# Performance work log

Measured on AMD Instinct MI355X. Metric: run time of the kernel, lower is better.

## Reference

```python
import jax, jax.numpy as jnp
import numpy as np

ARRAY_SIZE = 128   # crossbar rows
CBITS = 4          # psum ADC bits
LEV = 2 ** (CBITS - 1)
ALPHA = ARRAY_SIZE / LEV   # psum quant step
EPS = 1e-5

# ---- binary activation / weight quant with STE (hardtanh grad) ----
@jax.custom_vjp
def ste_sign(x):
    return jnp.where(x >= 0, 1.0, -1.0).astype(x.dtype)

def _sign_fwd(x):
    return ste_sign(x), x

def _sign_bwd(x, g):
    return (g * (jnp.abs(x) <= 1.0).astype(g.dtype),)

ste_sign.defvjp(_sign_fwd, _sign_bwd)

# ---- psum (partial-sum) quantization: cbits-level ADC over each crossbar array ----
@jax.custom_vjp
def psum_quant(p):
    return jnp.clip(jnp.round(p / ALPHA), -LEV, LEV - 1) * ALPHA

def _pq_fwd(p):
    return psum_quant(p), p

def _pq_bwd(p, g):
    return (g * (jnp.abs(p) <= ARRAY_SIZE).astype(g.dtype),)

psum_quant.defvjp(_pq_fwd, _pq_bwd)

# ---- layers ----
def bn(x, p):
    g, b, m, v = p  # each [C]
    sh = (1, -1) + (1,) * (x.ndim - 2)
    return (x - m.reshape(sh)) * (g.reshape(sh) / jnp.sqrt(v.reshape(sh) + EPS)) + b.reshape(sh)

def maxpool2(x):
    return jax.lax.reduce_window(x, -jnp.inf, jax.lax.max, (1, 1, 2, 2), (1, 1, 2, 2), 'VALID')

def conv_same(x, w):
    return jax.lax.conv_general_dilated(x, w, (1, 1), 'SAME')

def psum_conv(x, w):
    # crossbar-mapped conv: input channels split into groups of arraySize//(kh*kw),
    # each group conv'd separately, psum-quantized (ADC), then accumulated.
    O, Cin, kh, kw = w.shape
    chunk = max(1, ARRAY_SIZE // (kh * kw))
    G = -(-Cin // chunk)
    pad = G * chunk - Cin
    xp = jnp.pad(x, ((0, 0), (0, pad), (0, 0), (0, 0)))
    wp = jnp.pad(w, ((0, 0), (0, pad), (0, 0), (0, 0)))
    B, _, H, W = x.shape
    xg = xp.reshape(B, G, chunk, H, W).transpose(1, 0, 2, 3, 4)   # [G,B,c,H,W]
    wg = wp.reshape(O, G, chunk, kh, kw).transpose(1, 0, 2, 3, 4)  # [G,O,c,kh,kw]
    ps = jax.vmap(conv_same)(xg, wg)                               # [G,B,O,H,W]
    return psum_quant(ps).sum(0)

def psum_linear(x, w):
    # x [B,D], w [O,D]; D divisible by ARRAY_SIZE
    B, D = x.shape
    O = w.shape[0]
    G = D // ARRAY_SIZE
    ps = jnp.einsum('bgc,ogc->gbo', x.reshape(B, G, ARRAY_SIZE), w.reshape(O, G, ARRAY_SIZE))
    return psum_quant(ps).sum(0)


def setup_inputs() -> dict:
    key = jax.random.key(0)
    ks = iter(jax.random.split(key, 64))
    def nrm(shape, s=0.05):
        return jax.random.normal(next(ks), shape, jnp.float32) * s
    def bnp(C):
        return jnp.stack([jax.random.uniform(next(ks), (C,), jnp.float32) + 0.5,
                          nrm((C,), 0.1), nrm((C,), 0.1),
                          jax.random.uniform(next(ks), (C,), jnp.float32) + 0.5])
    return dict(
        x=jax.random.normal(next(ks), (64, 3, 32, 32), jnp.float32),
        conv0_w=nrm((128, 3, 3, 3)), bn0=bnp(128),
        w1=nrm((128, 128, 3, 3)), bn1=bnp(128),
        w2=nrm((256, 128, 3, 3)), bn2=bnp(256),
        w3=nrm((256, 256, 3, 3)), bn3=bnp(256),
        w4=nrm((512, 256, 3, 3)), bn4=bnp(512),
        w5=nrm((512, 512, 3, 3)), bn5=bnp(512),
        fc1_w=nrm((1024, 8192)), bnf1=bnp(1024),
        fc2_w=nrm((1024, 1024)), bnf2=bnp(1024),
        out_w=nrm((10, 1024)), out_b=nrm((10,)), bnout=bnp(10),
    )


def reference(x, conv0_w, bn0, w1, bn1, w2, bn2, w3, bn3, w4, bn4, w5, bn5,
              fc1_w, bnf1, fc2_w, bnf2, out_w, out_b, bnout):
    h = conv_same(x, conv0_w)                       # full-precision first conv
    h = ste_sign(bn(h, bn0))
    h = psum_conv(h, ste_sign(w1)); h = maxpool2(h); h = ste_sign(bn(h, bn1))
    h = psum_conv(h, ste_sign(w2)); h = ste_sign(bn(h, bn2))
    h = psum_conv(h, ste_sign(w3)); h = maxpool2(h); h = ste_sign(bn(h, bn3))
    h = psum_conv(h, ste_sign(w4)); h = ste_sign(bn(h, bn4))
    h = psum_conv(h, ste_sign(w5)); h = maxpool2(h); h = ste_sign(bn(h, bn5))
    h = h.reshape(h.shape[0], -1)                   # [B, 8192]
    h = ste_sign(bn(psum_linear(h, ste_sign(fc1_w)), bnf1))
    h = bn(psum_linear(h, ste_sign(fc2_w)), bnf2)   # abits=32 -> identity nonlinear
    h = h @ out_w.T + out_b
    return bn(h, bnout)
```

## Files before the change

kernel.cpp:

```cpp
#include <hip/hip_runtime.h>
#include <cstdint>
#include <cstddef>

using bf16x8 = __attribute__((ext_vector_type(8))) short;
using f32x4  = __attribute__((ext_vector_type(4))) float;
using u32x4  = __attribute__((ext_vector_type(4))) unsigned int;

#define DI __device__ __forceinline__

DI float pq16(float ps) {
    float q = rintf(ps * 0.0625f);
    q = fminf(7.f, fmaxf(-8.f, q));
    return q * 16.f;
}

DI float bnv(float x, float g, float b, float m, float v) {
    return (x - m) * (g / sqrtf(v + 1e-5f)) + b;
}

DI unsigned short sgn_bf16(float v) {
    return (v >= 0.f) ? (unsigned short)0x3F80 : (unsigned short)0xBF80;
}

__global__ __launch_bounds__(256)
void k_conv0(const float* __restrict__ x, const float* __restrict__ w,
             const float* __restrict__ bnp, unsigned short* __restrict__ out) {
    __shared__ float sX[3][3][36];
    const int b = blockIdx.x >> 5, y = blockIdx.x & 31;
    const int tid = threadIdx.x;
    const int o = tid & 127, xc = tid >> 7;

    for (int i = tid; i < 3 * 3 * 36; i += 256) {
        int col = i % 36, rr = (i / 36) % 3, c = i / 108;
        int gy = y + rr - 1, gx = col - 1;
        float v = 0.f;
        if ((unsigned)gy < 32u && (unsigned)gx < 32u)
            v = x[((b * 3 + c) * 32 + gy) * 32 + gx];
        sX[c][rr][col] = v;
    }
    float wr[27];
    const float* wp = w + o * 27;
    #pragma unroll
    for (int t = 0; t < 27; ++t) wr[t] = wp[t];
    __syncthreads();

    const float bg = bnp[o], bb = bnp[128 + o], bm = bnp[256 + o], bv = bnp[384 + o];
    unsigned short* op = out + ((size_t)(b * 32 + y) * 32) * 128 + o;

    #pragma unroll
    for (int q = 0; q < 4; ++q) {
        float acc0 = 0.f, acc1 = 0.f, acc2 = 0.f, acc3 = 0.f;
        const int X0 = xc * 16 + q * 4;
        #pragma unroll
        for (int c = 0; c < 3; ++c)
            #pragma unroll
            for (int ky = 0; ky < 3; ++ky) {
                float xv0 = sX[c][ky][X0 + 0], xv1 = sX[c][ky][X0 + 1];
                float xv2 = sX[c][ky][X0 + 2], xv3 = sX[c][ky][X0 + 3];
                float xv4 = sX[c][ky][X0 + 4], xv5 = sX[c][ky][X0 + 5];
                float w0 = wr[c * 9 + ky * 3 + 0];
                float w1 = wr[c * 9 + ky * 3 + 1];
                float w2 = wr[c * 9 + ky * 3 + 2];
                acc0 += xv0 * w0 + xv1 * w1 + xv2 * w2;
                acc1 += xv1 * w0 + xv2 * w1 + xv3 * w2;
                acc2 += xv2 * w0 + xv3 * w1 + xv4 * w2;
                acc3 += xv3 * w0 + xv4 * w1 + xv5 * w2;
            }
        op[(size_t)(X0 + 0) * 128] = sgn_bf16(bnv(acc0, bg, bb, bm, bv));
        op[(size_t)(X0 + 1) * 128] = sgn_bf16(bnv(acc1, bg, bb, bm, bv));
        op[(size_t)(X0 + 2) * 128] = sgn_bf16(bnv(acc2, bg, bb, bm, bv));
        op[(size_t)(X0 + 3) * 128] = sgn_bf16(bnv(acc3, bg, bb, bm, bv));
    }
}

__global__ __launch_bounds__(256)
void k_pack_w(const float* __restrict__ w, unsigned short* __restrict__ wpk,
              int Cin, int O, int G) {
    int idx = blockIdx.x * 256 + threadIdx.x;
    int total = G * O * 160;
    if (idx >= total) return;
    int c = idx & 15;
    int tap = (idx >> 4) % 10;
    int rest = idx / 160;
    int o = rest % O, g = rest / O;
    unsigned short v = 0;
    int cg = g * 14 + c;
    if (tap < 9 && c < 14 && cg < Cin)
        v = sgn_bf16(w[((size_t)o * Cin + cg) * 9 + tap]);
    wpk[idx] = v;
}

template <int H, int W, int Cin, int O, int G, int RH, int RW, int POOLMODE>
__global__ __launch_bounds__(256)
void k_conv_mfma(const unsigned int* __restrict__ act,
                 const unsigned short* __restrict__ wpk,
                 const float* __restrict__ bnp,
                 unsigned short* __restrict__ outa,
                 unsigned short* __restrict__ a5p) {
    constexpr int SH = RH + 2, SW = RW + 2;
    constexpr int MS = RH * RW / 16;
    constexpr int NREGX = W / RW;
    static_assert(POOLMODE != 1 || RW == 16, "pool mode 1 needs RW=16");
    static_assert(POOLMODE != 2 || (RW == 8 && MS == 4), "pool mode 2 needs 8x8");

    __shared__ __align__(16) unsigned int sA[SH * SW * 12];

    const int tid  = threadIdx.x;
    const int regY = (int)blockIdx.x / NREGX, regX = (int)blockIdx.x % NREGX;
    const int o0   = blockIdx.y * 64;
    const int b    = blockIdx.z;

    const int lane = tid & 63, wv = tid >> 6;
    const int n  = lane & 15;
    const int kb = lane >> 4;
    const int hb = kb >> 1, ch = kb & 1;

    int baseA[MS];
    #pragma unroll
    for (int ms = 0; ms < MS; ++ms) {
        int p = ms * 16 + n;
        int y = p / RW, x = p % RW;
        baseA[ms] = (y * SW + x) * 48 + ch * 16;
    }

    float tot[MS][4];
    #pragma unroll
    for (int ms = 0; ms < MS; ++ms) {
        tot[ms][0] = 0.f; tot[ms][1] = 0.f; tot[ms][2] = 0.f; tot[ms][3] = 0.f;
    }

    const unsigned short* wrow = wpk + ((size_t)o0 + wv * 16 + n) * 160 + ch * 8;

    #pragma unroll 1
    for (int g = 0; g < G; ++g) {
        const int rem_dw = (Cin - g * 14) >> 1;
        for (int i = tid; i < SH * SW * 8; i += 256) {
            int cp = i & 7, slot = i >> 3;
            int yy = slot / SW, xx = slot - yy * SW;
            int gy = regY * RH + yy - 1, gx = regX * RW + xx - 1;
            unsigned int v = 0;
            if (cp < 7 && cp < rem_dw &&
                (unsigned)gy < (unsigned)H && (unsigned)gx < (unsigned)W)
                v = act[(((size_t)b * H + gy) * W + gx) * (Cin / 2) + g * 7 + cp];
            sA[slot * 12 + cp] = v;
        }
        const unsigned short* wg = wrow + (size_t)g * O * 160;
        bf16x8 bq[5];
        #pragma unroll
        for (int s = 0; s < 5; ++s) {
            int tap = 2 * s + hb;
            bq[s] = *(const bf16x8*)(wg + tap * 16);
        }
        __syncthreads();

        const char* sAc = (const char*)sA;
        #pragma unroll
        for (int ms = 0; ms < MS; ++ms) {
            f32x4 acc = {0.f, 0.f, 0.f, 0.f};
            #pragma unroll
            for (int s = 0; s < 5; ++s) {
                const int t0 = 2 * s, t1 = 2 * s + 1;
                const int off0 = ((t0 / 3) * SW + (t0 % 3)) * 48;
                const int off1 = (t1 >= 9) ? 0 : ((t1 / 3) * SW + (t1 % 3)) * 48;
                int off = hb ? off1 : off0;
                bf16x8 af = *(const bf16x8*)(sAc + baseA[ms] + off);
                acc = __builtin_amdgcn_mfma_f32_16x16x32_bf16(af, bq[s], acc, 0, 0, 0);
            }
            tot[ms][0] += pq16(acc[0]);
            tot[ms][1] += pq16(acc[1]);
            tot[ms][2] += pq16(acc[2]);
            tot[ms][3] += pq16(acc[3]);
        }
        __syncthreads();
    }

    const int oc = o0 + wv * 16 + n;
    const float bg = bnp[oc], bb = bnp[O + oc], bm = bnp[2 * O + oc], bvr = bnp[3 * O + oc];

    if constexpr (POOLMODE == 0) {
        #pragma unroll
        for (int ms = 0; ms < MS; ++ms)
            #pragma unroll
            for (int r = 0; r < 4; ++r) {
                int p = ms * 16 + 4 * kb + r;
                int y = regY * RH + p / RW, x = regX * RW + p % RW;
                float val = bnv(tot[ms][r], bg, bb, bm, bvr);
                outa[(((size_t)b * H + y) * W + x) * O + oc] = sgn_bf16(val);
            }
    } else if constexpr (POOLMODE == 1) {
        #pragma unroll
        for (int j = 0; j < MS / 2; ++j)
            #pragma unroll
            for (int q = 0; q < 2; ++q) {
                float v = fmaxf(fmaxf(tot[2 * j][2 * q], tot[2 * j][2 * q + 1]),
                                fmaxf(tot[2 * j + 1][2 * q], tot[2 * j + 1][2 * q + 1]));
                float val = bnv(v, bg, bb, bm, bvr);
                int py = regY * (RH / 2) + j, px = regX * (RW / 2) + 2 * kb + q;
                outa[(((size_t)b * (H / 2) + py) * (W / 2) + px) * O + oc] = sgn_bf16(val);
            }
    } else {
        #pragma unroll
        for (int ms = 0; ms < MS; ++ms)
            #pragma unroll
            for (int q = 0; q < 2; ++q) {
                float h = fmaxf(tot[ms][2 * q], tot[ms][2 * q + 1]);
                float o2 = __shfl_xor(h, 32);
                float v = fmaxf(h, o2);
                if (hb == 0) {
                    float val = bnv(v, bg, bb, bm, bvr);
                    int d = oc * 16 + ms * 4 + 2 * ch + q;
                    a5p[((size_t)(d >> 3) * 64 + b) * 8 + (d & 7)] = sgn_bf16(val);
                }
            }
    }
}

template <int D, int GPB>
__global__ __launch_bounds__(256)
void k_fc_mfma(const unsigned short* __restrict__ bpk, const float* __restrict__ w,
               float* __restrict__ accg) {
    const int lane = threadIdx.x & 63, wv = threadIdx.x >> 6;
    const int n = lane & 15, kb = lane >> 4;
    const int orow = blockIdx.x * 64 + wv * 16 + n;
    const int g0 = blockIdx.y * GPB;

    float tot[4][4];
    #pragma unroll
    for (int s = 0; s < 4; ++s)
        #pragma unroll
        for (int r = 0; r < 4; ++r) tot[s][r] = 0.f;

    #pragma unroll 1
    for (int g = 0; g < GPB; ++g) {
        const int kbase = (g0 + g) * 128;
        f32x4 a0 = {0,0,0,0}, a1 = {0,0,0,0}, a2 = {0,0,0,0}, a3 = {0,0,0,0};
        #pragma unroll
        for (int s = 0; s < 4; ++s) {
            const int k0 = kbase + s * 32 + kb * 8;
            const float* wp = w + (size_t)orow * D + k0;
            float4 wlo = *(const float4*)wp;
            float4 whi = *(const float4*)(wp + 4);
            bf16x8 af;
            af[0] = (short)sgn_bf16(wlo.x); af[1] = (short)sgn_bf16(wlo.y);
            af[2] = (short)sgn_bf16(wlo.z); af[3] = (short)sgn_bf16(wlo.w);
            af[4] = (short)sgn_bf16(whi.x); af[5] = (short)sgn_bf16(whi.y);
            af[6] = (short)sgn_bf16(whi.z); af[7] = (short)sgn_bf16(whi.w);
            const unsigned short* bp = bpk + (size_t)(k0 >> 3) * 512;
            bf16x8 b0 = *(const bf16x8*)(bp + (n +  0) * 8);
            bf16x8 b1 = *(const bf16x8*)(bp + (n + 16) * 8);
            bf16x8 b2 = *(const bf16x8*)(bp + (n + 32) * 8);
            bf16x8 b3 = *(const bf16x8*)(bp + (n + 48) * 8);
            a0 = __builtin_amdgcn_mfma_f32_16x16x32_bf16(af, b0, a0, 0, 0, 0);
            a1 = __builtin_amdgcn_mfma_f32_16x16x32_bf16(af, b1, a1, 0, 0, 0);
            a2 = __builtin_amdgcn_mfma_f32_16x16x32_bf16(af, b2, a2, 0, 0, 0);
            a3 = __builtin_amdgcn_mfma_f32_16x16x32_bf16(af, b3, a3, 0, 0, 0);
        }
        #pragma unroll
        for (int r = 0; r < 4; ++r) {
            tot[0][r] += pq16(a0[r]); tot[1][r] += pq16(a1[r]);
            tot[2][r] += pq16(a2[r]); tot[3][r] += pq16(a3[r]);
        }
    }
    const int od = blockIdx.x * 64 + wv * 16 + kb * 4;
    #pragma unroll
    for (int s = 0; s < 4; ++s)
        #pragma unroll
        for (int r = 0; r < 4; ++r)
            atomicAdd(&accg[(size_t)(od + r) * 64 + s * 16 + n], tot[s][r]);
}

template <bool SIGN>
__global__ __launch_bounds__(256)
void k_fc_ep(const float* __restrict__ accg, const float* __restrict__ bnp,
             unsigned short* __restrict__ packed, float* __restrict__ h2, int O) {
    int idx = blockIdx.x * 256 + threadIdx.x;
    int b = idx & 63, o = idx >> 6;
    float val = bnv(accg[idx], bnp[o], bnp[O + o], bnp[2 * O + o], bnp[3 * O + o]);
    if (SIGN) packed[((size_t)(o >> 3) * 64 + b) * 8 + (o & 7)] = sgn_bf16(val);
    else      h2[(size_t)b * 1024 + o] = val;
}

__global__ __launch_bounds__(64)
void k_out(const float* __restrict__ h2, const float* __restrict__ ow,
           const float* __restrict__ ob, const float* __restrict__ bnp,
           float* __restrict__ out) {
    int b = blockIdx.x / 10, o = blockIdx.x % 10;
    int lane = threadIdx.x;
    float acc = 0.f;
    #pragma unroll
    for (int i = 0; i < 16; ++i) {
        int k = i * 64 + lane;
        acc += h2[b * 1024 + k] * ow[o * 1024 + k];
    }
    #pragma unroll
    for (int off = 32; off; off >>= 1) acc += __shfl_xor(acc, off);
    if (lane == 0)
        out[b * 10 + o] = bnv(acc + ob[o], bnp[o], bnp[10 + o], bnp[20 + o], bnp[30 + o]);
}

extern "C" void kernel_launch(void* const* d_in, const int* in_sizes, int n_in,
                              void* d_out, int out_size, void* d_ws, size_t ws_size,
                              hipStream_t stream) {
    const float* x     = (const float*)d_in[0];
    const float* w0    = (const float*)d_in[1];
    const float* bn0   = (const float*)d_in[2];
    const float* w1    = (const float*)d_in[3];
    const float* bn1   = (const float*)d_in[4];
    const float* w2    = (const float*)d_in[5];
    const float* bn2   = (const float*)d_in[6];
    const float* w3    = (const float*)d_in[7];
    const float* bn3   = (const float*)d_in[8];
    const float* w4    = (const float*)d_in[9];
    const float* bn4   = (const float*)d_in[10];
    const float* w5    = (const float*)d_in[11];
    const float* bn5   = (const float*)d_in[12];
    const float* fc1w  = (const float*)d_in[13];
    const float* bnf1  = (const float*)d_in[14];
    const float* fc2w  = (const float*)d_in[15];
    const float* bnf2  = (const float*)d_in[16];
    const float* outw  = (const float*)d_in[17];
    const float* outb  = (const float*)d_in[18];
    const float* bnout = (const float*)d_in[19];

    char* ws = (char*)d_ws;
    unsigned short* actA  = (unsigned short*)(ws);
    unsigned short* actB  = (unsigned short*)(ws + 16777216);
    unsigned short* wpk   = (unsigned short*)(ws + 20971520);
    unsigned short* a5p   = (unsigned short*)(ws + 27262976);
    unsigned short* a6p   = (unsigned short*)(ws + 28311552);
    float*          h1acc = (float*)(ws + 28442624);
    float*          h2acc = (float*)(ws + 28704768);
    float*          h2    = (float*)(ws + 28966912);

    const unsigned int* actA32 = (const unsigned int*)actA;
    const unsigned int* actB32 = (const unsigned int*)actB;

    hipMemsetAsync(h1acc, 0, 262144, stream);
    hipMemsetAsync(h2acc, 0, 262144, stream);

    k_conv0<<<dim3(2048), dim3(256), 0, stream>>>(x, w0, bn0, actA);

    k_pack_w<<<dim3(800), dim3(256), 0, stream>>>(w1, wpk, 128, 128, 10);
    k_conv_mfma<32, 32, 128, 128, 10, 8, 16, 1>
        <<<dim3(8, 2, 64), dim3(256), 0, stream>>>(actA32, wpk, bn1, actB, nullptr);

    k_pack_w<<<dim3(1600), dim3(256), 0, stream>>>(w2, wpk, 128, 256, 10);
    k_conv_mfma<16, 16, 128, 256, 10, 8, 16, 0>
        <<<dim3(2, 4, 64), dim3(256), 0, stream>>>(actB32, wpk, bn2, actA, nullptr);

    k_pack_w<<<dim3(3040), dim3(256), 0, stream>>>(w3, wpk, 256, 256, 19);
    k_conv_mfma<16, 16, 256, 256, 19, 8, 16, 1>
        <<<dim3(2, 4, 64), dim3(256), 0, stream>>>(actA32, wpk, bn3, actB, nullptr);

    k_pack_w<<<dim3(6080), dim3(256), 0, stream>>>(w4, wpk, 256, 512, 19);
    k_conv_mfma<8, 8, 256, 512, 19, 8, 8, 0>
        <<<dim3(1, 8, 64), dim3(256), 0, stream>>>(actB32, wpk, bn4, actA, nullptr);

    k_pack_w<<<dim3(11840), dim3(256), 0, stream>>>(w5, wpk, 512, 512, 37);
    k_conv_mfma<8, 8, 512, 512, 37, 8, 8, 2>
        <<<dim3(1, 8, 64), dim3(256), 0, stream>>>(actA32, wpk, bn5, nullptr, a5p);

    k_fc_mfma<8192, 4><<<dim3(16, 16), dim3(256), 0, stream>>>(a5p, fc1w, h1acc);
    k_fc_ep<true><<<dim3(256), dim3(256), 0, stream>>>(h1acc, bnf1, a6p, nullptr, 1024);

    k_fc_mfma<1024, 1><<<dim3(16, 8), dim3(256), 0, stream>>>(a6p, fc2w, h2acc);
    k_fc_ep<false><<<dim3(256), dim3(256), 0, stream>>>(h2acc, bnf2, nullptr, h2, 1024);

    k_out<<<dim3(640), dim3(64), 0, stream>>>(h2, outw, outb, bnout, (float*)d_out);
}
```

Before: 298.2 us.

## Split-K conv4/conv5 over crossbar groups with atomics, smaller tiles for conv2/conv3

Conv4 and conv5 now split their crossbar-group loop into chunks across extra blocks. Each chunk accumulates psum-quantized partials into a float buffer with atomicAdd, and separate epilogue kernels apply BN and sign, plus maxpool and packing for conv5. Conv2 and conv3 switch to 8x8 tiles, with conv3 gaining a new in-kernel 8x8 pooling mode, and FC1 uses finer group splitting. This raises block counts on the small-spatial layers to fill more compute units, at the cost of atomics, memsets of the partial buffer and extra epilogue launches.

```diff
diff --git a/kernel.cpp b/kernel.cpp
--- a/kernel.cpp
+++ b/kernel.cpp
@@ -90,25 +90,32 @@
     wpk[idx] = v;
 }
 
-template <int H, int W, int Cin, int O, int G, int RH, int RW, int POOLMODE>
+template <int H, int W, int Cin, int O, int RH, int RW, int POOLMODE>
 __global__ __launch_bounds__(256)
 void k_conv_mfma(const unsigned int* __restrict__ act,
                  const unsigned short* __restrict__ wpk,
                  const float* __restrict__ bnp,
                  unsigned short* __restrict__ outa,
-                 unsigned short* __restrict__ a5p) {
+                 unsigned short* __restrict__ a5p,
+                 float* __restrict__ Pacc,
+                 int gsz, int Gtot) {
     constexpr int SH = RH + 2, SW = RW + 2;
     constexpr int MS = RH * RW / 16;
     constexpr int NREGX = W / RW;
+    constexpr int NTILES = (H / RH) * (W / RW);
     static_assert(POOLMODE != 1 || RW == 16, "pool mode 1 needs RW=16");
-    static_assert(POOLMODE != 2 || (RW == 8 && MS == 4), "pool mode 2 needs 8x8");
+    static_assert((POOLMODE != 2 && POOLMODE != 4) || (RW == 8 && MS == 4), "modes 2/4 need 8x8");
 
     __shared__ __align__(16) unsigned int sA[SH * SW * 12];
 
     const int tid  = threadIdx.x;
-    const int regY = (int)blockIdx.x / NREGX, regX = (int)blockIdx.x % NREGX;
+    const int bx   = (int)blockIdx.x;
+    const int tile = bx % NTILES, chunk = bx / NTILES;
+    const int regY = tile / NREGX, regX = tile % NREGX;
     const int o0   = blockIdx.y * 64;
     const int b    = blockIdx.z;
+    const int g0   = chunk * gsz;
+    const int gend = min(g0 + gsz, Gtot);
 
     const int lane = tid & 63, wv = tid >> 6;
     const int n  = lane & 15;
@@ -132,7 +139,7 @@
     const unsigned short* wrow = wpk + ((size_t)o0 + wv * 16 + n) * 160 + ch * 8;
 
     #pragma unroll 1
-    for (int g = 0; g < G; ++g) {
+    for (int g = g0; g < gend; ++g) {
         const int rem_dw = (Cin - g * 14) >> 1;
         for (int i = tid; i < SH * SW * 8; i += 256) {
             int cp = i & 7, slot = i >> 3;
@@ -175,6 +182,19 @@
     }
 
     const int oc = o0 + wv * 16 + n;
+
+    if constexpr (POOLMODE == 3) {
+        #pragma unroll
+        for (int ms = 0; ms < MS; ++ms)
+            #pragma unroll
+            for (int r = 0; r < 4; ++r) {
+                int p = ms * 16 + 4 * kb + r;
+                int y = regY * RH + p / RW, x = regX * RW + p % RW;
+                atomicAdd(&Pacc[(((size_t)b * H + y) * W + x) * O + oc], tot[ms][r]);
+            }
+        return;
+    }
+
     const float bg = bnp[oc], bb = bnp[O + oc], bm = bnp[2 * O + oc], bvr = bnp[3 * O + oc];
 
     if constexpr (POOLMODE == 0) {
@@ -208,11 +228,40 @@
                 float v = fmaxf(h, o2);
                 if (hb == 0) {
                     float val = bnv(v, bg, bb, bm, bvr);
-                    int d = oc * 16 + ms * 4 + 2 * ch + q;
-                    a5p[((size_t)(d >> 3) * 64 + b) * 8 + (d & 7)] = sgn_bf16(val);
+                    int py = ms, px = 2 * ch + q;
+                    if constexpr (POOLMODE == 2) {
+                        int d = oc * 16 + py * 4 + px;
+                        a5p[((size_t)(d >> 3) * 64 + b) * 8 + (d & 7)] = sgn_bf16(val);
+                    } else {
+                        int gpy = regY * (RH / 2) + py, gpx = regX * (RW / 2) + px;
+                        outa[(((size_t)b * (H / 2) + gpy) * (W / 2) + gpx) * O + oc] = sgn_bf16(val);
+                    }
                 }
             }
     }
+}
+
+template <int O>
+__global__ __launch_bounds__(256)
+void k_ep_bnsign(const float* __restrict__ P, const float* __restrict__ bnp,
+                 unsigned short* __restrict__ outa) {
+    int idx = blockIdx.x * 256 + threadIdx.x;
+    int o = idx & (O - 1);
+    float val = bnv(P[idx], bnp[o], bnp[O + o], bnp[2 * O + o], bnp[3 * O + o]);
+    outa[idx] = sgn_bf16(val);
+}
+
+__global__ __launch_bounds__(256)
+void k_ep_pool_pack(const float* __restrict__ P, const float* __restrict__ bnp,
+                    unsigned short* __restrict__ a5p) {
+    int idx = blockIdx.x * 256 + threadIdx.x;
+    int o = idx & 511;
+    int px = (idx >> 9) & 3, py = (idx >> 11) & 3, b = idx >> 13;
+    const float* base = P + (((size_t)b * 8 + 2 * py) * 8 + 2 * px) * 512 + o;
+    float v = fmaxf(fmaxf(base[0], base[512]), fmaxf(base[8 * 512], base[8 * 512 + 512]));
+    float val = bnv(v, bnp[o], bnp[512 + o], bnp[1024 + o], bnp[1536 + o]);
+    int d = o * 16 + py * 4 + px;
+    a5p[((size_t)(d >> 3) * 64 + b) * 8 + (d & 7)] = sgn_bf16(val);
 }
 
 template <int D, int GPB>
@@ -326,11 +375,12 @@
     unsigned short* actA  = (unsigned short*)(ws);
     unsigned short* actB  = (unsigned short*)(ws + 16777216);
     unsigned short* wpk   = (unsigned short*)(ws + 20971520);
-    unsigned short* a5p   = (unsigned short*)(ws + 27262976);
-    unsigned short* a6p   = (unsigned short*)(ws + 28311552);
-    float*          h1acc = (float*)(ws + 28442624);
-    float*          h2acc = (float*)(ws + 28704768);
-    float*          h2    = (float*)(ws + 28966912);
+    float*          P     = (float*)(ws + 27262976);
+    unsigned short* a5p   = (unsigned short*)(ws + 35651584);
+    unsigned short* a6p   = (unsigned short*)(ws + 36700160);
+    float*          h1acc = (float*)(ws + 36831232);
+    float*          h2acc = (float*)(ws + 37093376);
+    float*          h2    = (float*)(ws + 37355520);
 
     const unsigned int* actA32 = (const unsigned int*)actA;
     const unsigned int* actB32 = (const unsigned int*)actB;
@@ -341,26 +391,30 @@
     k_conv0<<<dim3(2048), dim3(256), 0, stream>>>(x, w0, bn0, actA);
 
     k_pack_w<<<dim3(800), dim3(256), 0, stream>>>(w1, wpk, 128, 128, 10);
-    k_conv_mfma<32, 32, 128, 128, 10, 8, 16, 1>
-        <<<dim3(8, 2, 64), dim3(256), 0, stream>>>(actA32, wpk, bn1, actB, nullptr);
+    k_conv_mfma<32, 32, 128, 128, 8, 16, 1>
+        <<<dim3(8, 2, 64), dim3(256), 0, stream>>>(actA32, wpk, bn1, actB, nullptr, nullptr, 10, 10);
 
     k_pack_w<<<dim3(1600), dim3(256), 0, stream>>>(w2, wpk, 128, 256, 10);
-    k_conv_mfma<16, 16, 128, 256, 10, 8, 16, 0>
-        <<<dim3(2, 4, 64), dim3(256), 0, stream>>>(actB32, wpk, bn2, actA, nullptr);
+    k_conv_mfma<16, 16, 128, 256, 8, 8, 0>
+        <<<dim3(4, 4, 64), dim3(256), 0, stream>>>(actB32, wpk, bn2, actA, nullptr, nullptr, 10, 10);
 
     k_pack_w<<<dim3(3040), dim3(256), 0, stream>>>(w3, wpk, 256, 256, 19);
-    k_conv_mfma<16, 16, 256, 256, 19, 8, 16, 1>
-        <<<dim3(2, 4, 64), dim3(256), 0, stream>>>(actA32, wpk, bn3, actB, nullptr);
+    k_conv_mfma<16, 16, 256, 256, 8, 8, 4>
+        <<<dim3(4, 4, 64), dim3(256), 0, stream>>>(actA32, wpk, bn3, actB, nullptr, nullptr, 19, 19);
 
     k_pack_w<<<dim3(6080), dim3(256), 0, stream>>>(w4, wpk, 256, 512, 19);
-    k_conv_mfma<8, 8, 256, 512, 19, 8, 8, 0>
-        <<<dim3(1, 8, 64), dim3(256), 0, stream>>>(actB32, wpk, bn4, actA, nullptr);
+    hipMemsetAsync(P, 0, 8388608, stream);
+    k_conv_mfma<8, 8, 256, 512, 8, 8, 3>
+        <<<dim3(4, 8, 64), dim3(256), 0, stream>>>(actB32, wpk, nullptr, nullptr, nullptr, P, 5, 19);
+    k_ep_bnsign<512><<<dim3(8192), dim3(256), 0, stream>>>(P, bn4, actA);
 
     k_pack_w<<<dim3(11840), dim3(256), 0, stream>>>(w5, wpk, 512, 512, 37);
-    k_conv_mfma<8, 8, 512, 512, 37, 8, 8, 2>
-        <<<dim3(1, 8, 64), dim3(256), 0, stream>>>(actA32, wpk, bn5, nullptr, a5p);
-
-    k_fc_mfma<8192, 4><<<dim3(16, 16), dim3(256), 0, stream>>>(a5p, fc1w, h1acc);
+    hipMemsetAsync(P, 0, 8388608, stream);
+    k_conv_mfma<8, 8, 512, 512, 8, 8, 3>
+        <<<dim3(4, 8, 64), dim3(256), 0, stream>>>(actA32, wpk, nullptr, nullptr, nullptr, P, 10, 37);
+    k_ep_pool_pack<<<dim3(2048), dim3(256), 0, stream>>>(P, bn5, a5p);
+
+    k_fc_mfma<8192, 1><<<dim3(16, 64), dim3(256), 0, stream>>>(a5p, fc1w, h1acc);
     k_fc_ep<true><<<dim3(256), dim3(256), 0, stream>>>(h1acc, bnf1, a6p, nullptr, 1024);
 
     k_fc_mfma<1024, 1><<<dim3(16, 8), dim3(256), 0, stream>>>(a6p, fc2w, h2acc);
```

Result: slower. 321.1 us (+7.7%).

## Restructure binary convs to batch-as-M MFMA with blocked channel layout

Applied to the files above, without the earlier changes.

Replaces the spatial-tile conv kernel with one that maps batch into the MFMA M dimension and uses a channel-block-major activation layout, so each block loads fragments straight from global memory with no shared-memory staging or barriers. Each wave computes four 16-output tiles, which raises reuse of weight fragments. Weights are pre-scaled by 1/16 so the psum quant becomes a rint plus clamp, with the 16x folded into the epilogue. The last conv writes raw floats and a separate pool/BN kernel packs them for fc1, and fc1 is split into more groups. In exchange it uses more registers, adds an extra kernel and buffer, and reads activations directly from global memory where the shared-memory tiling used to provide reuse.

```diff
diff --git a/kernel.cpp b/kernel.cpp
--- a/kernel.cpp
+++ b/kernel.cpp
@@ -4,22 +4,18 @@
 
 using bf16x8 = __attribute__((ext_vector_type(8))) short;
 using f32x4  = __attribute__((ext_vector_type(4))) float;
-using u32x4  = __attribute__((ext_vector_type(4))) unsigned int;
 
 #define DI __device__ __forceinline__
-
-DI float pq16(float ps) {
-    float q = rintf(ps * 0.0625f);
-    q = fminf(7.f, fmaxf(-8.f, q));
-    return q * 16.f;
-}
 
 DI float bnv(float x, float g, float b, float m, float v) {
     return (x - m) * (g / sqrtf(v + 1e-5f)) + b;
 }
-
 DI unsigned short sgn_bf16(float v) {
     return (v >= 0.f) ? (unsigned short)0x3F80 : (unsigned short)0xBF80;
+}
+DI float pq_scaled(float a) {
+    float q = rintf(a);
+    return fminf(7.f, fmaxf(-8.f, q));
 }
 
 __global__ __launch_bounds__(256)
@@ -45,7 +41,10 @@
     __syncthreads();
 
     const float bg = bnp[o], bb = bnp[128 + o], bm = bnp[256 + o], bv = bnp[384 + o];
-    unsigned short* op = out + ((size_t)(b * 32 + y) * 32) * 128 + o;
+    const int cb0 = (o / 14) * 2 + ((o % 14) >> 3);
+    const int sl0 = (o % 14) & 7;
+    unsigned short* op = out + (size_t)(y * 32) * 10240 + (size_t)cb0 * 512
+                             + (size_t)b * 8 + sl0;
 
     #pragma unroll
     for (int q = 0; q < 4; ++q) {
@@ -66,10 +65,10 @@
                 acc2 += xv2 * w0 + xv3 * w1 + xv4 * w2;
                 acc3 += xv3 * w0 + xv4 * w1 + xv5 * w2;
             }
-        op[(size_t)(X0 + 0) * 128] = sgn_bf16(bnv(acc0, bg, bb, bm, bv));
-        op[(size_t)(X0 + 1) * 128] = sgn_bf16(bnv(acc1, bg, bb, bm, bv));
-        op[(size_t)(X0 + 2) * 128] = sgn_bf16(bnv(acc2, bg, bb, bm, bv));
-        op[(size_t)(X0 + 3) * 128] = sgn_bf16(bnv(acc3, bg, bb, bm, bv));
+        op[(size_t)(X0 + 0) * 10240] = sgn_bf16(bnv(acc0, bg, bb, bm, bv));
+        op[(size_t)(X0 + 1) * 10240] = sgn_bf16(bnv(acc1, bg, bb, bm, bv));
+        op[(size_t)(X0 + 2) * 10240] = sgn_bf16(bnv(acc2, bg, bb, bm, bv));
+        op[(size_t)(X0 + 3) * 10240] = sgn_bf16(bnv(acc3, bg, bb, bm, bv));
     }
 }
 
@@ -77,142 +76,156 @@
 void k_pack_w(const float* __restrict__ w, unsigned short* __restrict__ wpk,
               int Cin, int O, int G) {
     int idx = blockIdx.x * 256 + threadIdx.x;
-    int total = G * O * 160;
-    if (idx >= total) return;
-    int c = idx & 15;
-    int tap = (idx >> 4) % 10;
-    int rest = idx / 160;
-    int o = rest % O, g = rest / O;
+    if (idx >= G * O * 160) return;
+    int c8 = idx & 7;
+    int o  = (idx >> 3) % O;
+    int r2 = (idx >> 3) / O;
+    int chdw = r2 & 1, tap = (r2 >> 1) % 10, g = r2 / 20;
+    int c = chdw * 8 + c8, cg = g * 14 + c;
     unsigned short v = 0;
-    int cg = g * 14 + c;
     if (tap < 9 && c < 14 && cg < Cin)
-        v = sgn_bf16(w[((size_t)o * Cin + cg) * 9 + tap]);
+        v = (w[((size_t)o * Cin + cg) * 9 + tap] >= 0.f) ? (unsigned short)0x3D80
+                                                         : (unsigned short)0xBD80;
     wpk[idx] = v;
 }
 
-template <int H, int W, int Cin, int O, int G, int RH, int RW, int POOLMODE>
-__global__ __launch_bounds__(256)
-void k_conv_mfma(const unsigned int* __restrict__ act,
-                 const unsigned short* __restrict__ wpk,
-                 const float* __restrict__ bnp,
-                 unsigned short* __restrict__ outa,
-                 unsigned short* __restrict__ a5p) {
-    constexpr int SH = RH + 2, SW = RW + 2;
-    constexpr int MS = RH * RW / 16;
-    constexpr int NREGX = W / RW;
-    static_assert(POOLMODE != 1 || RW == 16, "pool mode 1 needs RW=16");
-    static_assert(POOLMODE != 2 || (RW == 8 && MS == 4), "pool mode 2 needs 8x8");
-
-    __shared__ __align__(16) unsigned int sA[SH * SW * 12];
-
-    const int tid  = threadIdx.x;
-    const int regY = (int)blockIdx.x / NREGX, regX = (int)blockIdx.x % NREGX;
-    const int o0   = blockIdx.y * 64;
-    const int b    = blockIdx.z;
-
-    const int lane = tid & 63, wv = tid >> 6;
-    const int n  = lane & 15;
-    const int kb = lane >> 4;
-    const int hb = kb >> 1, ch = kb & 1;
-
-    int baseA[MS];
+template <int H, int W, int CB, int O, int G, int MS, int OUTMODE, int OUTCB, int MINW>
+__global__ __launch_bounds__(256, MINW)
+void k_conv_bm(const char* __restrict__ act, const char* __restrict__ wpk,
+               const float* __restrict__ bnp, unsigned short* __restrict__ outa,
+               float* __restrict__ P) {
+    static_assert(OUTMODE != 1 || MS == 4, "pool mode needs quad");
+    const int tid = threadIdx.x;
+    const int lane = tid & 63, bg = tid >> 6;
+    const int n = lane & 15, kb = lane >> 4, hb = kb >> 1, chdw = kb & 1;
+    const int sp = blockIdx.x;
+    const int o0 = blockIdx.y * 64;
+
+    int pix[MS];
+    int qY = 0, qX = 0;
+    if constexpr (MS == 4) {
+        qY = sp / (W / 2); qX = sp % (W / 2);
+        #pragma unroll
+        for (int ms = 0; ms < 4; ++ms)
+            pix[ms] = (2 * qY + (ms >> 1)) * W + 2 * qX + (ms & 1);
+    } else {
+        pix[0] = sp;
+    }
+
+    const int bl = (bg * 16 + n) * 16 + chdw * 1024;
+    int off[MS][5];
     #pragma unroll
     for (int ms = 0; ms < MS; ++ms) {
-        int p = ms * 16 + n;
-        int y = p / RW, x = p % RW;
-        baseA[ms] = (y * SW + x) * 48 + ch * 16;
-    }
-
-    float tot[MS][4];
-    #pragma unroll
-    for (int ms = 0; ms < MS; ++ms) {
-        tot[ms][0] = 0.f; tot[ms][1] = 0.f; tot[ms][2] = 0.f; tot[ms][3] = 0.f;
-    }
-
-    const unsigned short* wrow = wpk + ((size_t)o0 + wv * 16 + n) * 160 + ch * 8;
+        int py = pix[ms] / W, px = pix[ms] % W;
+        #pragma unroll
+        for (int s = 0; s < 5; ++s) {
+            int t = 2 * s + hb;
+            int ty = t / 3, tx = t - 3 * ty;
+            int gy = py + ty - 1, gx = px + tx - 1;
+            bool valid = (t <= 8) && ((unsigned)gy < (unsigned)H) && ((unsigned)gx < (unsigned)W);
+            off[ms][s] = valid ? ((gy * W + gx) * CB) * 1024 + bl : (int)0xC0000000;
+        }
+    }
+
+    const char* wl = wpk + (size_t)(((hb * 2 + chdw) * O) + o0 + n) * 16;
+
+    float tot[MS][4][4];
+    #pragma unroll
+    for (int ms = 0; ms < MS; ++ms)
+        #pragma unroll
+        for (int nt = 0; nt < 4; ++nt)
+            #pragma unroll
+            for (int r = 0; r < 4; ++r) tot[ms][nt][r] = 0.f;
+
+    const bf16x8 az = {0, 0, 0, 0, 0, 0, 0, 0};
 
     #pragma unroll 1
     for (int g = 0; g < G; ++g) {
-        const int rem_dw = (Cin - g * 14) >> 1;
-        for (int i = tid; i < SH * SW * 8; i += 256) {
-            int cp = i & 7, slot = i >> 3;
-            int yy = slot / SW, xx = slot - yy * SW;
-            int gy = regY * RH + yy - 1, gx = regX * RW + xx - 1;
-            unsigned int v = 0;
-            if (cp < 7 && cp < rem_dw &&
-                (unsigned)gy < (unsigned)H && (unsigned)gx < (unsigned)W)
-                v = act[(((size_t)b * H + gy) * W + gx) * (Cin / 2) + g * 7 + cp];
-            sA[slot * 12 + cp] = v;
-        }
-        const unsigned short* wg = wrow + (size_t)g * O * 160;
-        bf16x8 bq[5];
+        f32x4 acc[MS][4];
+        #pragma unroll
+        for (int ms = 0; ms < MS; ++ms)
+            #pragma unroll
+            for (int nt = 0; nt < 4; ++nt) acc[ms][nt] = (f32x4){0.f, 0.f, 0.f, 0.f};
+
+        const char* wg = wl + (size_t)g * (20 * O * 16);
+        const char* ag = act + (size_t)g * 2048;
         #pragma unroll
         for (int s = 0; s < 5; ++s) {
-            int tap = 2 * s + hb;
-            bq[s] = *(const bf16x8*)(wg + tap * 16);
-        }
-        __syncthreads();
-
-        const char* sAc = (const char*)sA;
-        #pragma unroll
-        for (int ms = 0; ms < MS; ++ms) {
-            f32x4 acc = {0.f, 0.f, 0.f, 0.f};
-            #pragma unroll
-            for (int s = 0; s < 5; ++s) {
-                const int t0 = 2 * s, t1 = 2 * s + 1;
-                const int off0 = ((t0 / 3) * SW + (t0 % 3)) * 48;
-                const int off1 = (t1 >= 9) ? 0 : ((t1 / 3) * SW + (t1 % 3)) * 48;
-                int off = hb ? off1 : off0;
-                bf16x8 af = *(const bf16x8*)(sAc + baseA[ms] + off);
-                acc = __builtin_amdgcn_mfma_f32_16x16x32_bf16(af, bq[s], acc, 0, 0, 0);
+            bf16x8 bq[4];
+            #pragma unroll
+            for (int nt = 0; nt < 4; ++nt)
+                bq[nt] = *(const bf16x8*)(wg + s * (4 * O * 16) + nt * 256);
+            #pragma unroll
+            for (int ms = 0; ms < MS; ++ms) {
+                bf16x8 af = az;
+                int ofs = off[ms][s];
+                if (ofs >= 0) af = *(const bf16x8*)(ag + ofs);
+                #pragma unroll
+                for (int nt = 0; nt < 4; ++nt)
+                    acc[ms][nt] = __builtin_amdgcn_mfma_f32_16x16x32_bf16(af, bq[nt], acc[ms][nt], 0, 0, 0);
             }
-            tot[ms][0] += pq16(acc[0]);
-            tot[ms][1] += pq16(acc[1]);
-            tot[ms][2] += pq16(acc[2]);
-            tot[ms][3] += pq16(acc[3]);
-        }
-        __syncthreads();
-    }
-
-    const int oc = o0 + wv * 16 + n;
-    const float bg = bnp[oc], bb = bnp[O + oc], bm = bnp[2 * O + oc], bvr = bnp[3 * O + oc];
-
-    if constexpr (POOLMODE == 0) {
+        }
         #pragma unroll
         for (int ms = 0; ms < MS; ++ms)
             #pragma unroll
+            for (int nt = 0; nt < 4; ++nt)
+                #pragma unroll
+                for (int r = 0; r < 4; ++r)
+                    tot[ms][nt][r] += pq_scaled(acc[ms][nt][r]);
+    }
+
+    const int bb = bg * 16 + kb * 4;
+    if constexpr (OUTMODE == 2) {
+        #pragma unroll
+        for (int nt = 0; nt < 4; ++nt) {
+            int oc = o0 + nt * 16 + n;
+            #pragma unroll
+            for (int r = 0; r < 4; ++r)
+                P[((size_t)pix[0] * 512 + oc) * 64 + bb + r] = tot[0][nt][r];
+        }
+    } else {
+        #pragma unroll
+        for (int nt = 0; nt < 4; ++nt) {
+            int oc = o0 + nt * 16 + n;
+            float g_ = bnp[oc], b_ = bnp[O + oc], m_ = bnp[2 * O + oc], v_ = bnp[3 * O + oc];
+            int q14 = oc / 14, r14 = oc - 14 * q14;
+            int cb = 2 * q14 + (r14 >> 3), sl = r14 & 7;
+            int ppos = (OUTMODE == 1) ? (qY * (W / 2) + qX) : pix[0];
+            #pragma unroll
             for (int r = 0; r < 4; ++r) {
-                int p = ms * 16 + 4 * kb + r;
-                int y = regY * RH + p / RW, x = regX * RW + p % RW;
-                float val = bnv(tot[ms][r], bg, bb, bm, bvr);
-                outa[(((size_t)b * H + y) * W + x) * O + oc] = sgn_bf16(val);
+                float v;
+                if constexpr (OUTMODE == 1)
+                    v = fmaxf(fmaxf(tot[0][nt][r], tot[1][nt][r]),
+                              fmaxf(tot[2][nt][r], tot[3][nt][r]));
+                else
+                    v = tot[0][nt][r];
+                float val = bnv(16.f * v, g_, b_, m_, v_);
+                outa[((size_t)ppos * OUTCB + cb) * 512 + (size_t)(bb + r) * 8 + sl] = sgn_bf16(val);
             }
-    } else if constexpr (POOLMODE == 1) {
-        #pragma unroll
-        for (int j = 0; j < MS / 2; ++j)
-            #pragma unroll
-            for (int q = 0; q < 2; ++q) {
-                float v = fmaxf(fmaxf(tot[2 * j][2 * q], tot[2 * j][2 * q + 1]),
-                                fmaxf(tot[2 * j + 1][2 * q], tot[2 * j + 1][2 * q + 1]));
-                float val = bnv(v, bg, bb, bm, bvr);
-                int py = regY * (RH / 2) + j, px = regX * (RW / 2) + 2 * kb + q;
-                outa[(((size_t)b * (H / 2) + py) * (W / 2) + px) * O + oc] = sgn_bf16(val);
-            }
-    } else {
-        #pragma unroll
-        for (int ms = 0; ms < MS; ++ms)
-            #pragma unroll
-            for (int q = 0; q < 2; ++q) {
-                float h = fmaxf(tot[ms][2 * q], tot[ms][2 * q + 1]);
-                float o2 = __shfl_xor(h, 32);
-                float v = fmaxf(h, o2);
-                if (hb == 0) {
-                    float val = bnv(v, bg, bb, bm, bvr);
-                    int d = oc * 16 + ms * 4 + 2 * ch + q;
-                    a5p[((size_t)(d >> 3) * 64 + b) * 8 + (d & 7)] = sgn_bf16(val);
-                }
-            }
-    }
+        }
+    }
+}
+
+__global__ __launch_bounds__(256)
+void k_ep_pool5(const float* __restrict__ P, const float* __restrict__ bnp,
+                unsigned short* __restrict__ a5p) {
+    int idx = blockIdx.x * 256 + threadIdx.x;
+    int b = idx & 63;
+    int o = (idx >> 6) & 511;
+    int pq = idx >> 15;
+    int py = pq >> 2, px = pq & 3;
+    const float* p0 = P + ((size_t)(2 * py * 8 + 2 * px) * 512 + o) * 64 + b;
+    const int dx = 512 * 64, dy = 8 * 512 * 64;
+    float v = fmaxf(fmaxf(p0[0], p0[dx]), fmaxf(p0[dy], p0[dy + dx]));
+    float val = bnv(16.f * v, bnp[o], bnp[512 + o], bnp[1024 + o], bnp[1536 + o]);
+    int d = o * 16 + py * 4 + px;
+    a5p[((size_t)(d >> 3) * 64 + b) * 8 + (d & 7)] = sgn_bf16(val);
+}
+
+DI float pq16(float ps) {
+    float q = rintf(ps * 0.0625f);
+    q = fminf(7.f, fmaxf(-8.f, q));
+    return q * 16.f;
 }
 
 template <int D, int GPB>
@@ -323,48 +336,46 @@
     const float* bnout = (const float*)d_in[19];
 
     char* ws = (char*)d_ws;
-    unsigned short* actA  = (unsigned short*)(ws);
-    unsigned short* actB  = (unsigned short*)(ws + 16777216);
-    unsigned short* wpk   = (unsigned short*)(ws + 20971520);
-    unsigned short* a5p   = (unsigned short*)(ws + 27262976);
-    unsigned short* a6p   = (unsigned short*)(ws + 28311552);
-    float*          h1acc = (float*)(ws + 28442624);
-    float*          h2acc = (float*)(ws + 28704768);
-    float*          h2    = (float*)(ws + 28966912);
-
-    const unsigned int* actA32 = (const unsigned int*)actA;
-    const unsigned int* actB32 = (const unsigned int*)actB;
+    char*           ping  = ws;
+    char*           pong  = ws + 20971520;
+    unsigned short* wpk   = (unsigned short*)(ws + 26214400);
+    float*          P     = (float*)(ws + 32505856);
+    unsigned short* a5p   = (unsigned short*)(ws + 40894464);
+    unsigned short* a6p   = (unsigned short*)(ws + 41943040);
+    float*          h1acc = (float*)(ws + 42074112);
+    float*          h2acc = (float*)(ws + 42336256);
+    float*          h2    = (float*)(ws + 42598400);
+    const char*     wpkc  = (const char*)wpk;
 
     hipMemsetAsync(h1acc, 0, 262144, stream);
     hipMemsetAsync(h2acc, 0, 262144, stream);
 
-    k_conv0<<<dim3(2048), dim3(256), 0, stream>>>(x, w0, bn0, actA);
+    k_conv0<<<dim3(2048), dim3(256), 0, stream>>>(x, w0, bn0, (unsigned short*)ping);
 
     k_pack_w<<<dim3(800), dim3(256), 0, stream>>>(w1, wpk, 128, 128, 10);
-    k_conv_mfma<32, 32, 128, 128, 10, 8, 16, 1>
-        <<<dim3(8, 2, 64), dim3(256), 0, stream>>>(actA32, wpk, bn1, actB, nullptr);
+    k_conv_bm<32, 32, 20, 128, 10, 4, 1, 20, 2>
+        <<<dim3(256, 2), dim3(256), 0, stream>>>(ping, wpkc, bn1, (unsigned short*)pong, nullptr);
 
     k_pack_w<<<dim3(1600), dim3(256), 0, stream>>>(w2, wpk, 128, 256, 10);
-    k_conv_mfma<16, 16, 128, 256, 10, 8, 16, 0>
-        <<<dim3(2, 4, 64), dim3(256), 0, stream>>>(actB32, wpk, bn2, actA, nullptr);
+    k_conv_bm<16, 16, 20, 256, 10, 1, 0, 38, 4>
+        <<<dim3(256, 4), dim3(256), 0, stream>>>(pong, wpkc, bn2, (unsigned short*)ping, nullptr);
 
     k_pack_w<<<dim3(3040), dim3(256), 0, stream>>>(w3, wpk, 256, 256, 19);
-    k_conv_mfma<16, 16, 256, 256, 19, 8, 16, 1>
-        <<<dim3(2, 4, 64), dim3(256), 0, stream>>>(actA32, wpk, bn3, actB, nullptr);
+    k_conv_bm<16, 16, 38, 256, 19, 4, 1, 38, 2>
+        <<<dim3(64, 4), dim3(256), 0, stream>>>(ping, wpkc, bn3, (unsigned short*)pong, nullptr);
 
     k_pack_w<<<dim3(6080), dim3(256), 0, stream>>>(w4, wpk, 256, 512, 19);
-    k_conv_mfma<8, 8, 256, 512, 19, 8, 8, 0>
-        <<<dim3(1, 8, 64), dim3(256), 0, stream>>>(actB32, wpk, bn4, actA, nullptr);
+    k_conv_bm<8, 8, 38, 512, 19, 1, 0, 74, 4>
+        <<<dim3(64, 8), dim3(256), 0, stream>>>(pong, wpkc, bn4, (unsigned short*)ping, nullptr);
 
     k_pack_w<<<dim3(11840), dim3(256), 0, stream>>>(w5, wpk, 512, 512, 37);
-    k_conv_mfma<8, 8, 512, 512, 37, 8, 8, 2>
-        <<<dim3(1, 8, 64), dim3(256), 0, stream>>>(actA32, wpk, bn5, nullptr, a5p);
-
-    k_fc_mfma<8192, 4><<<dim3(16, 16), dim3(256), 0, stream>>>(a5p, fc1w, h1acc);
+    k_conv_bm<8, 8, 74, 512, 37, 1, 2, 1, 4>
+        <<<dim3(64, 8), dim3(256), 0, stream>>>(ping, wpkc, nullptr, nullptr, P);
+    k_ep_pool5<<<dim3(2048), dim3(256), 0, stream>>>(P, bn5, a5p);
+
+    k_fc_mfma<8192, 1><<<dim3(16, 64), dim3(256), 0, stream>>>(a5p, fc1w, h1acc);
     k_fc_ep<true><<<dim3(256), dim3(256), 0, stream>>>(h1acc, bnf1, a6p, nullptr, 1024);
-
     k_fc_mfma<1024, 1><<<dim3(16, 8), dim3(256), 0, stream>>>(a6p, fc2w, h2acc);
     k_fc_ep<false><<<dim3(256), dim3(256), 0, stream>>>(h2acc, bnf2, nullptr, h2, 1024);
-
     k_out<<<dim3(640), dim3(64), 0, stream>>>(h2, outw, outb, bnout, (float*)d_out);
 }
```

Result: slower. 354.7 us (+18.9%).

## Add dedicated 8x8 conv kernel for layers 4-5 with padded channel layout and split-group passes

Applied to the files above, without the earlier changes.

Adds a new conv kernel for the 8x8 layers (conv4, conv5). Each block stages a whole image's padded activation tile in shared memory and uses 16x16x32 bf16 MFMAs with a new weight packing that pre-scales signs by 1/16. The group loop is split across two launches that pass fp32 partial sums through a workspace buffer, with the BN, sign and pool epilogue in the second pass. Layer-3 output is written in a 14-channel-padded layout so the group chunks line up, and fc1 now uses more grid blocks with one group per block. The intent is better occupancy and data reuse on the small spatial layers. In exchange it adds extra launches and the global round-trip of the partial sums.

```diff
diff --git a/kernel.cpp b/kernel.cpp
--- a/kernel.cpp
+++ b/kernel.cpp
@@ -12,6 +12,10 @@
     float q = rintf(ps * 0.0625f);
     q = fminf(7.f, fmaxf(-8.f, q));
     return q * 16.f;
+}
+DI float pq_scaled(float a) {
+    float q = rintf(a);
+    return fminf(7.f, fmaxf(-8.f, q));
 }
 
 DI float bnv(float x, float g, float b, float m, float v) {
@@ -90,18 +94,33 @@
     wpk[idx] = v;
 }
 
-template <int H, int W, int Cin, int O, int G, int RH, int RW, int POOLMODE>
+__global__ __launch_bounds__(256)
+void k_pack_w2(const float* __restrict__ w, unsigned short* __restrict__ wpk,
+               int Cin, int O, int G) {
+    int idx = blockIdx.x * 256 + threadIdx.x;
+    if (idx >= G * O * 160) return;
+    int c8 = idx & 7;
+    int o  = (idx >> 3) % O;
+    int r2 = (idx >> 3) / O;
+    int chdw = r2 & 1, tap = (r2 >> 1) % 10, g = r2 / 20;
+    int c = chdw * 8 + c8, cg = g * 14 + c;
+    unsigned short v = 0;
+    if (tap < 9 && c < 14 && cg < Cin)
+        v = (w[((size_t)o * Cin + cg) * 9 + tap] >= 0.f) ? (unsigned short)0x3D80
+                                                         : (unsigned short)0xBD80;
+    wpk[idx] = v;
+}
+
+template <int H, int W, int Cin, int O, int G, int RH, int RW, int POOLMODE, int PADC>
 __global__ __launch_bounds__(256)
 void k_conv_mfma(const unsigned int* __restrict__ act,
                  const unsigned short* __restrict__ wpk,
                  const float* __restrict__ bnp,
-                 unsigned short* __restrict__ outa,
-                 unsigned short* __restrict__ a5p) {
+                 unsigned short* __restrict__ outa) {
     constexpr int SH = RH + 2, SW = RW + 2;
     constexpr int MS = RH * RW / 16;
     constexpr int NREGX = W / RW;
     static_assert(POOLMODE != 1 || RW == 16, "pool mode 1 needs RW=16");
-    static_assert(POOLMODE != 2 || (RW == 8 && MS == 4), "pool mode 2 needs 8x8");
 
     __shared__ __align__(16) unsigned int sA[SH * SW * 12];
 
@@ -187,7 +206,7 @@
                 float val = bnv(tot[ms][r], bg, bb, bm, bvr);
                 outa[(((size_t)b * H + y) * W + x) * O + oc] = sgn_bf16(val);
             }
-    } else if constexpr (POOLMODE == 1) {
+    } else {
         #pragma unroll
         for (int j = 0; j < MS / 2; ++j)
             #pragma unroll
@@ -196,22 +215,129 @@
                                 fmaxf(tot[2 * j + 1][2 * q], tot[2 * j + 1][2 * q + 1]));
                 float val = bnv(v, bg, bb, bm, bvr);
                 int py = regY * (RH / 2) + j, px = regX * (RW / 2) + 2 * kb + q;
-                outa[(((size_t)b * (H / 2) + py) * (W / 2) + px) * O + oc] = sgn_bf16(val);
-            }
-    } else {
-        #pragma unroll
-        for (int ms = 0; ms < MS; ++ms)
-            #pragma unroll
-            for (int q = 0; q < 2; ++q) {
-                float h = fmaxf(tot[ms][2 * q], tot[ms][2 * q + 1]);
-                float o2 = __shfl_xor(h, 32);
-                float v = fmaxf(h, o2);
-                if (hb == 0) {
-                    float val = bnv(v, bg, bb, bm, bvr);
-                    int d = oc * 16 + ms * 4 + 2 * ch + q;
-                    a5p[((size_t)(d >> 3) * 64 + b) * 8 + (d & 7)] = sgn_bf16(val);
+                if constexpr (PADC == 0) {
+                    outa[(((size_t)b * (H / 2) + py) * (W / 2) + px) * O + oc] = sgn_bf16(val);
+                } else {
+                    int cidx = oc + 2 * (oc / 14);
+                    outa[(((size_t)b * (H / 2) + py) * (W / 2) + px) * PADC + cidx] = sgn_bf16(val);
                 }
             }
+    }
+}
+
+template <int O, int G0, int G1, int INB, int SPITCH, int PASS, int EPI, int NEXTC>
+__global__ __launch_bounds__(256, 2)
+void k_conv3(const char* __restrict__ act, const char* __restrict__ wpk2,
+             const float* __restrict__ bnp, float* __restrict__ P,
+             unsigned short* __restrict__ outa, unsigned short* __restrict__ a5p) {
+    constexpr int NV = (G1 - G0) * 2;
+    __shared__ __align__(16) char sA[100 * SPITCH];
+
+    const int tid  = threadIdx.x;
+    const int lane = tid & 63, wv = tid >> 6;
+    const int n = lane & 15, kb = lane >> 4, hb = kb >> 1, chdw = kb & 1;
+    const int img = blockIdx.x;
+    const int o0  = blockIdx.y * 64;
+
+    for (int i = tid; i < 100 * NV; i += 256) {
+        int slot = i / NV, v = i - slot * NV;
+        int yy = slot / 10, xx = slot - yy * 10;
+        int gy = yy - 1, gx = xx - 1;
+        u32x4 val = {0, 0, 0, 0};
+        if ((unsigned)gy < 8u && (unsigned)gx < 8u)
+            val = *(const u32x4*)(act + (size_t)(img * 64 + gy * 8 + gx) * INB
+                                      + G0 * 32 + v * 16);
+        *(u32x4*)(sA + slot * SPITCH + v * 16) = val;
+    }
+    __syncthreads();
+
+    const int px16 = wv * 16 + n;
+    const int ay = px16 >> 3, ax = px16 & 7;
+    int offA[5];
+    #pragma unroll
+    for (int s = 0; s < 5; ++s) {
+        int t = 2 * s + hb;
+        int slot = (t > 8) ? 0 : ((ay + t / 3) * 10 + ax + t % 3);
+        offA[s] = slot * SPITCH + chdw * 16;
+    }
+
+    const char* wl = wpk2 + (size_t)(o0 + n) * 16 + (size_t)chdw * (O * 16);
+
+    float tot[4][4];
+    #pragma unroll
+    for (int nt = 0; nt < 4; ++nt)
+        #pragma unroll
+        for (int r = 0; r < 4; ++r) tot[nt][r] = 0.f;
+
+    #pragma unroll 1
+    for (int g = G0; g < G1; ++g) {
+        f32x4 a0 = {0,0,0,0}, a1 = {0,0,0,0}, a2 = {0,0,0,0}, a3 = {0,0,0,0};
+        const char* sag = sA + (g - G0) * 32;
+        const char* wgg = wl + (size_t)g * (20 * O * 16);
+        #pragma unroll
+        for (int s = 0; s < 5; ++s) {
+            int t = 2 * s + hb;
+            const char* wt = wgg + (size_t)t * (2 * O * 16);
+            bf16x8 b0 = *(const bf16x8*)(wt);
+            bf16x8 b1 = *(const bf16x8*)(wt + 256);
+            bf16x8 b2 = *(const bf16x8*)(wt + 512);
+            bf16x8 b3 = *(const bf16x8*)(wt + 768);
+            bf16x8 af = *(const bf16x8*)(sag + offA[s]);
+            a0 = __builtin_amdgcn_mfma_f32_16x16x32_bf16(af, b0, a0, 0, 0, 0);
+            a1 = __builtin_amdgcn_mfma_f32_16x16x32_bf16(af, b1, a1, 0, 0, 0);
+            a2 = __builtin_amdgcn_mfma_f32_16x16x32_bf16(af, b2, a2, 0, 0, 0);
+            a3 = __builtin_amdgcn_mfma_f32_16x16x32_bf16(af, b3, a3, 0, 0, 0);
+        }
+        #pragma unroll
+        for (int r = 0; r < 4; ++r) {
+            tot[0][r] += pq_scaled(a0[r]); tot[1][r] += pq_scaled(a1[r]);
+            tot[2][r] += pq_scaled(a2[r]); tot[3][r] += pq_scaled(a3[r]);
+        }
+    }
+
+    const int pxd = wv * 16 + 4 * kb;
+    if constexpr (PASS == 0) {
+        #pragma unroll
+        for (int nt = 0; nt < 4; ++nt)
+            #pragma unroll
+            for (int r = 0; r < 4; ++r)
+                P[(size_t)(img * 64 + pxd + r) * O + o0 + nt * 16 + n] = tot[nt][r];
+    } else {
+        #pragma unroll
+        for (int nt = 0; nt < 4; ++nt)
+            #pragma unroll
+            for (int r = 0; r < 4; ++r)
+                tot[nt][r] += P[(size_t)(img * 64 + pxd + r) * O + o0 + nt * 16 + n];
+        if constexpr (EPI == 0) {
+            #pragma unroll
+            for (int nt = 0; nt < 4; ++nt) {
+                int oc = o0 + nt * 16 + n;
+                float g_ = bnp[oc], b_ = bnp[O + oc], m_ = bnp[2 * O + oc], v_ = bnp[3 * O + oc];
+                int cidx = oc + 2 * (oc / 14);
+                #pragma unroll
+                for (int r = 0; r < 4; ++r) {
+                    float val = bnv(16.f * tot[nt][r], g_, b_, m_, v_);
+                    outa[(size_t)(img * 64 + pxd + r) * NEXTC + cidx] = sgn_bf16(val);
+                }
+            }
+        } else {
+            #pragma unroll
+            for (int nt = 0; nt < 4; ++nt) {
+                int oc = o0 + nt * 16 + n;
+                float g_ = bnp[oc], b_ = bnp[O + oc], m_ = bnp[2 * O + oc], v_ = bnp[3 * O + oc];
+                #pragma unroll
+                for (int q = 0; q < 2; ++q) {
+                    float h = fmaxf(tot[nt][2 * q], tot[nt][2 * q + 1]);
+                    float o2 = __shfl_xor(h, 32);
+                    if (hb == 0) {
+                        float v = fmaxf(h, o2);
+                        float val = bnv(16.f * v, g_, b_, m_, v_);
+                        int d = oc * 16 + wv * 4 + 2 * kb + q;
+                        a5p[((size_t)(d >> 3) * 64 + img) * 8 + (d & 7)] = sgn_bf16(val);
+                    }
+                }
+            }
+        }
     }
 }
 
@@ -326,14 +452,18 @@
     unsigned short* actA  = (unsigned short*)(ws);
     unsigned short* actB  = (unsigned short*)(ws + 16777216);
     unsigned short* wpk   = (unsigned short*)(ws + 20971520);
-    unsigned short* a5p   = (unsigned short*)(ws + 27262976);
-    unsigned short* a6p   = (unsigned short*)(ws + 28311552);
-    float*          h1acc = (float*)(ws + 28442624);
-    float*          h2acc = (float*)(ws + 28704768);
-    float*          h2    = (float*)(ws + 28966912);
+    unsigned short* actC  = (unsigned short*)(ws + 27262976);
+    unsigned short* actD  = (unsigned short*)(ws + 29753344);
+    float*          P     = (float*)(ws + 34603008);
+    unsigned short* a5p   = (unsigned short*)(ws + 42991616);
+    unsigned short* a6p   = (unsigned short*)(ws + 44040192);
+    float*          h1acc = (float*)(ws + 44171264);
+    float*          h2acc = (float*)(ws + 44433408);
+    float*          h2    = (float*)(ws + 44695552);
 
     const unsigned int* actA32 = (const unsigned int*)actA;
     const unsigned int* actB32 = (const unsigned int*)actB;
+    const char* wpkc = (const char*)wpk;
 
     hipMemsetAsync(h1acc, 0, 262144, stream);
     hipMemsetAsync(h2acc, 0, 262144, stream);
@@ -341,30 +471,32 @@
     k_conv0<<<dim3(2048), dim3(256), 0, stream>>>(x, w0, bn0, actA);
 
     k_pack_w<<<dim3(800), dim3(256), 0, stream>>>(w1, wpk, 128, 128, 10);
-    k_conv_mfma<32, 32, 128, 128, 10, 8, 16, 1>
-        <<<dim3(8, 2, 64), dim3(256), 0, stream>>>(actA32, wpk, bn1, actB, nullptr);
+    k_conv_mfma<32, 32, 128, 128, 10, 8, 16, 1, 0>
+        <<<dim3(8, 2, 64), dim3(256), 0, stream>>>(actA32, wpk, bn1, actB);
 
     k_pack_w<<<dim3(1600), dim3(256), 0, stream>>>(w2, wpk, 128, 256, 10);
-    k_conv_mfma<16, 16, 128, 256, 10, 8, 16, 0>
-        <<<dim3(2, 4, 64), dim3(256), 0, stream>>>(actB32, wpk, bn2, actA, nullptr);
+    k_conv_mfma<16, 16, 128, 256, 10, 8, 16, 0, 0>
+        <<<dim3(2, 4, 64), dim3(256), 0, stream>>>(actB32, wpk, bn2, actA);
 
     k_pack_w<<<dim3(3040), dim3(256), 0, stream>>>(w3, wpk, 256, 256, 19);
-    k_conv_mfma<16, 16, 256, 256, 19, 8, 16, 1>
-        <<<dim3(2, 4, 64), dim3(256), 0, stream>>>(actA32, wpk, bn3, actB, nullptr);
-
-    k_pack_w<<<dim3(6080), dim3(256), 0, stream>>>(w4, wpk, 256, 512, 19);
-    k_conv_mfma<8, 8, 256, 512, 19, 8, 8, 0>
-        <<<dim3(1, 8, 64), dim3(256), 0, stream>>>(actB32, wpk, bn4, actA, nullptr);
-
-    k_pack_w<<<dim3(11840), dim3(256), 0, stream>>>(w5, wpk, 512, 512, 37);
-    k_conv_mfma<8, 8, 512, 512, 37, 8, 8, 2>
-        <<<dim3(1, 8, 64), dim3(256), 0, stream>>>(actA32, wpk, bn5, nullptr, a5p);
-
-    k_fc_mfma<8192, 4><<<dim3(16, 16), dim3(256), 0, stream>>>(a5p, fc1w, h1acc);
+    k_conv_mfma<16, 16, 256, 256, 19, 8, 16, 1, 304>
+        <<<dim3(2, 4, 64), dim3(256), 0, stream>>>(actA32, wpk, bn3, actC);
+
+    k_pack_w2<<<dim3(6080), dim3(256), 0, stream>>>(w4, wpk, 256, 512, 19);
+    k_conv3<512, 0, 10, 608, 336, 0, 0, 592>
+        <<<dim3(64, 8), dim3(256), 0, stream>>>((const char*)actC, wpkc, nullptr, P, nullptr, nullptr);
+    k_conv3<512, 10, 19, 608, 304, 1, 0, 592>
+        <<<dim3(64, 8), dim3(256), 0, stream>>>((const char*)actC, wpkc, bn4, P, actD, nullptr);
+
+    k_pack_w2<<<dim3(11840), dim3(256), 0, stream>>>(w5, wpk, 512, 512, 37);
+    k_conv3<512, 0, 19, 1184, 624, 0, 1, 0>
+        <<<dim3(64, 8), dim3(256), 0, stream>>>((const char*)actD, wpkc, nullptr, P, nullptr, nullptr);
+    k_conv3<512, 19, 37, 1184, 592, 1, 1, 0>
+        <<<dim3(64, 8), dim3(256), 0, stream>>>((const char*)actD, wpkc, bn5, P, nullptr, a5p);
+
+    k_fc_mfma<8192, 1><<<dim3(16, 64), dim3(256), 0, stream>>>(a5p, fc1w, h1acc);
     k_fc_ep<true><<<dim3(256), dim3(256), 0, stream>>>(h1acc, bnf1, a6p, nullptr, 1024);
-
     k_fc_mfma<1024, 1><<<dim3(16, 8), dim3(256), 0, stream>>>(a6p, fc2w, h2acc);
     k_fc_ep<false><<<dim3(256), dim3(256), 0, stream>>>(h2acc, bnf2, nullptr, h2, 1024);
-
     k_out<<<dim3(640), dim3(64), 0, stream>>>(h2, outw, outb, bnout, (float*)d_out);
 }
```

Result: slower. 342.4 us (+14.8%).
